# Performance work log

Hardware: AMD Instinct MI355X
Metric: run time of the kernel (lower is better)

The kernel has to match this reference:

```python
import jax, jax.numpy as jnp
import numpy as np

DIM = 1024
HID = 4096
NH = 16
HD = DIM // NH
B, S = 4, 2048
EPS = 1e-5
NEG = -1e9  # stand-in for -inf causal mask fill (numerically safe)


def layer_norm(x, g, b):
    mu = jnp.mean(x, axis=-1, keepdims=True)
    var = jnp.mean((x - mu) ** 2, axis=-1, keepdims=True)
    return (x - mu) * jax.lax.rsqrt(var + EPS) * g + b


def setup_inputs() -> dict:
    key = jax.random.key(0)
    ks = jax.random.split(key, 8)
    x = jax.random.normal(ks[0], (B, S, DIM), dtype=jnp.float32)
    # causal additive mask, broadcastable to [B, NH, S, S]
    causal = jnp.tril(jnp.ones((S, S), dtype=bool))
    mask = jnp.where(causal, 0.0, NEG).astype(jnp.float32)[None, None]
    sc = 1.0 / np.sqrt(DIM)
    wq = jax.random.normal(ks[1], (DIM, DIM), dtype=jnp.float32) * sc
    wk = jax.random.normal(ks[2], (DIM, DIM), dtype=jnp.float32) * sc
    wv = jax.random.normal(ks[3], (DIM, DIM), dtype=jnp.float32) * sc
    wo = jax.random.normal(ks[4], (DIM, DIM), dtype=jnp.float32) * sc
    w1 = jax.random.normal(ks[5], (DIM, HID), dtype=jnp.float32) * sc
    w2 = jax.random.normal(ks[6], (HID, DIM), dtype=jnp.float32) * (1.0 / np.sqrt(HID))
    ln1_w = jnp.ones((DIM,), jnp.float32); ln1_b = jnp.zeros((DIM,), jnp.float32)
    ln2_w = jnp.ones((DIM,), jnp.float32); ln2_b = jnp.zeros((DIM,), jnp.float32)
    return {"x": x, "mask": mask, "wq": wq, "wk": wk, "wv": wv, "wo": wo,
            "w1": w1, "w2": w2, "ln1_w": ln1_w, "ln1_b": ln1_b,
            "ln2_w": ln2_w, "ln2_b": ln2_b}


def reference(x, mask, wq, wk, wv, wo, w1, w2, ln1_w, ln1_b, ln2_w, ln2_b):
    b, s, _ = x.shape
    # pre-norm attention
    xn = layer_norm(x, ln1_w, ln1_b)
    q = (xn @ wq).reshape(b, s, NH, HD)
    k = (xn @ wk).reshape(b, s, NH, HD)
    v = (xn @ wv).reshape(b, s, NH, HD)
    scores = jnp.einsum('bqhd,bkhd->bhqk', q, k) / np.sqrt(HD) + mask
    probs = jax.nn.softmax(scores.astype(jnp.float32), axis=-1).astype(x.dtype)
    attn = jnp.einsum('bhqk,bkhd->bqhd', probs, v).reshape(b, s, NH * HD)
    h = x + attn @ wo
    # pre-norm ReLU FFN
    hn = layer_norm(h, ln2_w, ln2_b)
    ff = jax.nn.relu((hn @ w1).astype(jnp.float32)).astype(x.dtype) @ w2
    return h + ff
```

## Files before the change

kernel.cpp:

```cpp
#include <hip/hip_runtime.h>
#include <hip/hip_bf16.h>
#include <type_traits>

#define DIM 1024
#define HID 4096
#define NH 16
#define HD 64
#define BB 4
#define SS 2048
#define NROW (BB*SS)

typedef __attribute__((ext_vector_type(8))) short short8;
typedef __attribute__((ext_vector_type(4))) short short4v;
typedef __attribute__((ext_vector_type(4))) float f32x4;

__device__ __forceinline__ void gload16(const void* src, void* lds) {
  __builtin_amdgcn_global_load_lds(
      (const __attribute__((address_space(1))) unsigned int*)src,
      (__attribute__((address_space(3))) unsigned int*)lds, 16, 0, 0);
}
__device__ __forceinline__ short f2b(float f) {
  return __builtin_bit_cast(short, __float2bfloat16(f));
}
__device__ __forceinline__ float b2f(short s) {
  return __uint_as_float(((unsigned)(unsigned short)s) << 16);
}

__global__ __launch_bounds__(256) void ln_k(const float* __restrict__ x,
                                            const float* __restrict__ g,
                                            const float* __restrict__ bta,
                                            short* __restrict__ out) {
  int row = blockIdx.x;
  int t = threadIdx.x;
  int lane = t & 63, wid = t >> 6;
  float4 v = *(const float4*)(x + (size_t)row*DIM + t*4);
  float f[4] = {v.x, v.y, v.z, v.w};
  float s1 = 0.f, s2 = 0.f;
#pragma unroll
  for (int j = 0; j < 4; j++) { s1 += f[j]; s2 += f[j]*f[j]; }
#pragma unroll
  for (int off = 32; off > 0; off >>= 1) { s1 += __shfl_xor(s1, off); s2 += __shfl_xor(s2, off); }
  __shared__ float red[8];
  if (lane == 0) { red[wid] = s1; red[4+wid] = s2; }
  __syncthreads();
  s1 = red[0]+red[1]+red[2]+red[3];
  s2 = red[4]+red[5]+red[6]+red[7];
  float mu = s1 * (1.0f/DIM);
  float var = s2 * (1.0f/DIM) - mu*mu;
  float rs = rsqrtf(var + 1e-5f);
  float4 gv = *(const float4*)(g + t*4);
  float4 bv = *(const float4*)(bta + t*4);
  short4v o;
  o[0] = f2b((f[0]-mu)*rs*gv.x + bv.x);
  o[1] = f2b((f[1]-mu)*rs*gv.y + bv.y);
  o[2] = f2b((f[2]-mu)*rs*gv.z + bv.z);
  o[3] = f2b((f[3]-mu)*rs*gv.w + bv.w);
  *(short4v*)(out + (size_t)row*DIM + t*4) = o;
}

__global__ __launch_bounds__(256) void transp_f2b(const float* __restrict__ in, short* __restrict__ out,
                                                  int R, int C) {
  __shared__ __align__(16) short tile[64][72];
  int r0 = blockIdx.x*64, c0 = blockIdx.y*64;
  int t = threadIdx.x;
  int cr = t >> 4;
  int cc4 = (t & 15) * 4;
#pragma unroll
  for (int i = 0; i < 4; i++) {
    float4 v = *(const float4*)(in + (size_t)(r0 + cr + i*16)*C + c0 + cc4);
    tile[cr + i*16][cc4 + 0] = f2b(v.x);
    tile[cr + i*16][cc4 + 1] = f2b(v.y);
    tile[cr + i*16][cc4 + 2] = f2b(v.z);
    tile[cr + i*16][cc4 + 3] = f2b(v.w);
  }
  __syncthreads();
  int rr = t >> 3, cc = (t & 7) * 8;
#pragma unroll
  for (int i = 0; i < 2; i++) {
    int oc = rr + i*32;
    short8 v;
#pragma unroll
    for (int j = 0; j < 8; j++) v[j] = tile[cc + j][oc];
    *(short8*)(out + (size_t)(c0 + oc)*R + r0 + cc) = v;
  }
}

__global__ __launch_bounds__(256) void transp_f2b4(const float* __restrict__ w0, const float* __restrict__ w1,
                                                   const float* __restrict__ w2, const float* __restrict__ w3,
                                                   short* __restrict__ o0, short* __restrict__ o1,
                                                   short* __restrict__ o2, short* __restrict__ o3) {
  __shared__ __align__(16) short tile[64][72];
  int zz = blockIdx.z;
  const float* in = (zz == 0) ? w0 : (zz == 1) ? w1 : (zz == 2) ? w2 : w3;
  short* out = (zz == 0) ? o0 : (zz == 1) ? o1 : (zz == 2) ? o2 : o3;
  const int R = DIM, C = DIM;
  int r0 = blockIdx.x*64, c0 = blockIdx.y*64;
  int t = threadIdx.x;
  int cr = t >> 4;
  int cc4 = (t & 15) * 4;
#pragma unroll
  for (int i = 0; i < 4; i++) {
    float4 v = *(const float4*)(in + (size_t)(r0 + cr + i*16)*C + c0 + cc4);
    tile[cr + i*16][cc4 + 0] = f2b(v.x);
    tile[cr + i*16][cc4 + 1] = f2b(v.y);
    tile[cr + i*16][cc4 + 2] = f2b(v.z);
    tile[cr + i*16][cc4 + 3] = f2b(v.w);
  }
  __syncthreads();
  int rr = t >> 3, cc = (t & 7) * 8;
#pragma unroll
  for (int i = 0; i < 2; i++) {
    int oc = rr + i*32;
    short8 v;
#pragma unroll
    for (int j = 0; j < 8; j++) v[j] = tile[cc + j][oc];
    *(short8*)(out + (size_t)(c0 + oc)*R + r0 + cc) = v;
  }
}

__global__ __launch_bounds__(256) void vtrans(const short* __restrict__ qkv, short* __restrict__ vt) {
  __shared__ __align__(16) short tile[64][72];
  int s0 = blockIdx.x*64;
  int z = blockIdx.y; int b = z >> 4, h = z & 15;
  int t = threadIdx.x;
  int rr = t >> 3, cc = (t & 7) * 8;
#pragma unroll
  for (int i = 0; i < 2; i++) {
    short8 v = *(const short8*)(qkv + (size_t)(b*SS + s0 + rr + i*32)*(3*DIM) + 2*DIM + h*HD + cc);
    *(short8*)&tile[rr + i*32][cc] = v;
  }
  __syncthreads();
#pragma unroll
  for (int i = 0; i < 2; i++) {
    int d = rr + i*32;
    short8 v;
#pragma unroll
    for (int j = 0; j < 8; j++) v[j] = tile[cc + j][d];
    *(short8*)(vt + ((size_t)z*HD + d)*SS + s0 + cc) = v;
  }
}

template<int EPI, typename CT>
__global__ __launch_bounds__(512) void gemm_bt(const short* __restrict__ A, int lda,
                                               const short* __restrict__ Bt, int ldb,
                                               CT* C, int ldc,
                                               const float* Res, int ldr,
                                               int K) {
  __shared__ __align__(16) short ldsA[128*128];
  __shared__ __align__(16) short ldsB[128*128];
  int t = threadIdx.x, lane = t & 63, wid = t >> 6;
  int bm = blockIdx.x*128, bn = blockIdx.y*128;
  int wr = wid >> 2, wc = wid & 3;
  f32x4 z4 = {0.f, 0.f, 0.f, 0.f};
  f32x4 acc[4][2];
#pragma unroll
  for (int m = 0; m < 4; m++)
#pragma unroll
    for (int n = 0; n < 2; n++) acc[m][n] = z4;
  const int srcCol = (((t & 15) ^ ((t >> 4) & 15)) * 8);
  const short* pa = A + (size_t)(bm + (t >> 4))*lda + srcCol;
  const short* pb = Bt + (size_t)(bn + (t >> 4))*ldb + srcCol;
  const int rdXor = (lane & 15) << 3;
  for (int k0 = 0; k0 < K; k0 += 128) {
#pragma unroll
    for (int i = 0; i < 4; i++) {
      gload16(pa + (size_t)(i*32)*lda, &ldsA[i*4096 + wid*512]);
      gload16(pb + (size_t)(i*32)*ldb, &ldsB[i*4096 + wid*512]);
    }
    pa += 128; pb += 128;
    __syncthreads();
#pragma unroll
    for (int kk = 0; kk < 4; kk++) {
      short8 af[4], bfr[2];
#pragma unroll
      for (int m = 0; m < 4; m++) {
        int row = wr*64 + m*16 + (lane & 15);
        af[m] = *(const short8*)&ldsA[row*128 + ((kk*32 + (lane >> 4)*8) ^ rdXor)];
      }
#pragma unroll
      for (int n = 0; n < 2; n++) {
        int row = wc*32 + n*16 + (lane & 15);
        bfr[n] = *(const short8*)&ldsB[row*128 + ((kk*32 + (lane >> 4)*8) ^ rdXor)];
      }
#pragma unroll
      for (int m = 0; m < 4; m++)
#pragma unroll
        for (int n = 0; n < 2; n++)
          acc[m][n] = __builtin_amdgcn_mfma_f32_16x16x32_bf16(af[m], bfr[n], acc[m][n], 0, 0, 0);
    }
    __syncthreads();
  }
#pragma unroll
  for (int m = 0; m < 4; m++) {
    int r0 = bm + wr*64 + m*16 + ((lane >> 4) << 2);
#pragma unroll
    for (int n = 0; n < 2; n++) {
      int c = bn + wc*32 + n*16 + (lane & 15);
#pragma unroll
      for (int r = 0; r < 4; r++) {
        float v = acc[m][n][r];
        if constexpr (EPI == 1) v = fmaxf(v, 0.0f);
        if constexpr (EPI == 3) v += Res[(size_t)(r0 + r)*ldr + c];
        if constexpr (std::is_same<CT, float>::value)
          C[(size_t)(r0 + r)*ldc + c] = v;
        else
          C[(size_t)(r0 + r)*ldc + c] = f2b(v);
      }
    }
  }
}

__global__ __launch_bounds__(512) void attn_k(short* qkv, const short* __restrict__ vt) {
  __shared__ __align__(16) short ldsK[2][64*64];
  __shared__ __align__(16) short ldsV[2][64*64];
  __shared__ __align__(16) short ldsP[8][16*64];
  int t = threadIdx.x, lane = t & 63, wid = t >> 6;
  int wgid = blockIdx.x;
  int xcd = wgid & 7, idx = wgid >> 3;
  int z  = xcd*8 + (idx & 7);
  int p  = idx >> 3;
  int qiA = 15 - p, qiB = p;
  int b = z >> 4, h = z & 15;
  const int ld = 3*DIM;
  const float SCALE2 = 0.125f * 1.44269504f;
  const float THR2   = 8.0f * 1.44269504f;
  const int half = wid >> 2;
  const int nA = 2*qiA + 2;
  const int NT = 34;

  short8 qf[2];
  f32x4 z4 = {0.f, 0.f, 0.f, 0.f};
  f32x4 accO[4];
  float m_r[4], lp[4];
  const int srcCol = (((lane & 7) ^ ((lane >> 3) & 7)) * 8);
  const int rowXor = (lane & 7) << 3;

  auto LOADQ = [&](int q0) {
    const short* qp = qkv + (size_t)(b*SS + q0 + wid*16 + (lane & 15))*ld + h*HD + (lane >> 4)*8;
    qf[0] = *(const short8*)qp;
    qf[1] = *(const short8*)(qp + 32);
  };
  auto RESET = [&]() {
#pragma unroll
    for (int n = 0; n < 4; n++) accO[n] = z4;
#pragma unroll
    for (int r = 0; r < 4; r++) { m_r[r] = -1e30f; lp[r] = 0.f; }
  };
  auto EPILOG = [&](int q0e) {
    float rl[4];
#pragma unroll
    for (int r = 0; r < 4; r++) {
      float l = lp[r];
#pragma unroll
      for (int off = 1; off < 16; off <<= 1) l += __shfl_xor(l, off);
      rl[r] = 1.0f / l;
    }
#pragma unroll
    for (int nn = 0; nn < 4; nn++)
#pragma unroll
      for (int r = 0; r < 4; r++) {
        int qg = q0e + wid*16 + ((lane >> 4) << 2) + r;
        qkv[(size_t)(b*SS + qg)*ld + 2*DIM + h*HD + nn*16 + (lane & 15)] = f2b(accO[nn][r] * rl[r]);
      }
  };
  auto STAGE = [&](int kv0, int bsel) {
    const short* sk = qkv + (size_t)(b*SS + kv0 + (t >> 3))*ld + DIM + h*HD + srcCol;
    gload16(sk, &ldsK[bsel][wid*512]);
    const short* sv = vt + ((size_t)z*HD + (t >> 3))*SS + kv0 + srcCol;
    gload16(sv, &ldsV[bsel][wid*512]);
  };

  LOADQ(qiA*128);
  RESET();
  int qi = qiA, q0 = qiA*128;
  STAGE(0, 0);
  __syncthreads();
  for (int v = 0; v < NT; ++v) {
    int cur = v & 1;
    if (v + 1 < NT) {
      int vn = v + 1;
      STAGE(((vn >= nA) ? vn - nA : vn) * 64, cur ^ 1);
    }
    if (v == nA) {
      EPILOG(q0);
      RESET();
      qi = qiB; q0 = qiB*128;
      LOADQ(q0);
    }
    int it = (v >= nA) ? v - nA : v;
    int kv0 = it*64;
    if (it <= 2*qi + half) {
      f32x4 sacc[4];
#pragma unroll
      for (int n = 0; n < 4; n++) sacc[n] = z4;
      __builtin_amdgcn_s_setprio(1);
#pragma unroll
      for (int n = 0; n < 4; n++) {
#pragma unroll
        for (int kk = 0; kk < 2; kk++) {
          int colK = (kk*32 + (lane >> 4)*8) ^ rowXor;
          short8 kb = *(const short8*)&ldsK[cur][(n*16 + (lane & 15))*64 + colK];
          sacc[n] = __builtin_amdgcn_mfma_f32_16x16x32_bf16(qf[kk], kb, sacc[n], 0, 0, 0);
        }
      }
      __builtin_amdgcn_s_setprio(0);
      if (it == 2*qi + half) {
#pragma unroll
        for (int n = 0; n < 4; n++) {
          int kg = kv0 + n*16 + (lane & 15);
#pragma unroll
          for (int r = 0; r < 4; r++) {
            int qg = q0 + wid*16 + ((lane >> 4) << 2) + r;
            sacc[n][r] = (kg <= qg) ? sacc[n][r] : -1e30f;
          }
        }
      }
      float mxs[4];
      float dmax = -1e30f;
#pragma unroll
      for (int r = 0; r < 4; r++) {
        float mx = fmaxf(fmaxf(sacc[0][r], sacc[1][r]), fmaxf(sacc[2][r], sacc[3][r]));
#pragma unroll
        for (int off = 1; off < 16; off <<= 1) mx = fmaxf(mx, __shfl_xor(mx, off));
        mxs[r] = mx * SCALE2;
        dmax = fmaxf(dmax, mxs[r] - m_r[r]);
      }
      if (__any(dmax > THR2)) {
#pragma unroll
        for (int r = 0; r < 4; r++) {
          float mn = fmaxf(m_r[r], mxs[r]);
          float al = exp2f(m_r[r] - mn);
          m_r[r] = mn;
          lp[r] *= al;
#pragma unroll
          for (int n = 0; n < 4; n++) accO[n][r] *= al;
        }
      }
#pragma unroll
      for (int r = 0; r < 4; r++) {
        float mn = m_r[r];
        float rs = 0.f;
#pragma unroll
        for (int n = 0; n < 4; n++) {
          float p2 = exp2f(fmaf(sacc[n][r], SCALE2, -mn));
          sacc[n][r] = p2;
          rs += p2;
        }
        lp[r] += rs;
      }
#pragma unroll
      for (int n = 0; n < 4; n++)
#pragma unroll
        for (int r = 0; r < 4; r++) {
          int prow = ((lane >> 4) << 2) + r;
          int pcol = (n*16 + (lane & 15)) ^ ((prow & 7) << 3);
          ldsP[wid][prow*64 + pcol] = f2b(sacc[n][r]);
        }
      __builtin_amdgcn_s_setprio(1);
#pragma unroll
      for (int nn = 0; nn < 4; nn++) {
#pragma unroll
        for (int kk = 0; kk < 2; kk++) {
          int colP = (kk*32 + (lane >> 4)*8) ^ rowXor;
          short8 vb  = *(const short8*)&ldsV[cur][(nn*16 + (lane & 15))*64 + colP];
          short8 pfr = *(const short8*)&ldsP[wid][(lane & 15)*64 + colP];
          accO[nn] = __builtin_amdgcn_mfma_f32_16x16x32_bf16(pfr, vb, accO[nn], 0, 0, 0);
        }
      }
      __builtin_amdgcn_s_setprio(0);
    }
    __syncthreads();
  }
  EPILOG(q0);
}

extern "C" void kernel_launch(void* const* d_in, const int* in_sizes, int n_in,
                              void* d_out, int out_size, void* d_ws, size_t ws_size,
                              hipStream_t stream) {
  (void)in_sizes; (void)n_in; (void)out_size; (void)ws_size;
  const float* x    = (const float*)d_in[0];
  const float* wq   = (const float*)d_in[2];
  const float* wk   = (const float*)d_in[3];
  const float* wv   = (const float*)d_in[4];
  const float* wo   = (const float*)d_in[5];
  const float* w1   = (const float*)d_in[6];
  const float* w2   = (const float*)d_in[7];
  const float* ln1w = (const float*)d_in[8];
  const float* ln1b = (const float*)d_in[9];
  const float* ln2w = (const float*)d_in[10];
  const float* ln2b = (const float*)d_in[11];
  float* out = (float*)d_out;

  short* ws = (short*)d_ws;
  size_t o = 0;
  short* wqkvT = ws + o; o += (size_t)3*DIM*DIM;
  short* woT   = ws + o; o += (size_t)DIM*DIM;
  short* w1T   = ws + o; o += (size_t)HID*DIM;
  short* w2T   = ws + o; o += (size_t)DIM*HID;
  short* xn    = ws + o; o += (size_t)NROW*DIM;
  short* qkv   = ws + o; o += (size_t)NROW*3*DIM;
  short* ff1   = ws + o; o += (size_t)NROW*HID;
  short* vtb   = ff1;

  dim3 B256(256), B512(512);
  transp_f2b4<<<dim3(16,16,4), B256, 0, stream>>>(wq, wk, wv, wo,
                                                  wqkvT, wqkvT + DIM*DIM, wqkvT + 2*DIM*DIM, woT);
  transp_f2b<<<dim3(16,64), B256, 0, stream>>>(w1, w1T, DIM, HID);
  transp_f2b<<<dim3(64,16), B256, 0, stream>>>(w2, w2T, HID, DIM);
  ln_k<<<NROW, B256, 0, stream>>>(x, ln1w, ln1b, xn);
  gemm_bt<0, short><<<dim3(NROW/128, 3*DIM/128), B512, 0, stream>>>(xn, DIM, wqkvT, DIM, qkv, 3*DIM, nullptr, 0, DIM);
  vtrans<<<dim3(SS/64, BB*NH), B256, 0, stream>>>(qkv, vtb);
  attn_k<<<dim3(512), B512, 0, stream>>>(qkv, vtb);
  gemm_bt<3, float><<<dim3(NROW/128, DIM/128), B512, 0, stream>>>(qkv + 2*DIM, 3*DIM, woT, DIM, out, DIM, x, DIM, DIM);
  ln_k<<<NROW, B256, 0, stream>>>(out, ln2w, ln2b, xn);
  gemm_bt<1, short><<<dim3(NROW/128, HID/128), B512, 0, stream>>>(xn, DIM, w1T, DIM, ff1, HID, nullptr, 0, DIM);
  gemm_bt<3, float><<<dim3(NROW/128, DIM/128), B512, 0, stream>>>(ff1, HID, w2T, HID, out, DIM, out, DIM, HID);
}
```

Measured before the change: 385.0 us.

## Widen attention KV tile to 128 with per-wave diagonal causal masking

Doubles the KV block staged per iteration from 64 to 128 keys, halving the loop trip count and the number of block-wide barriers per query tile. All waves now process every KV block; on the diagonal block, waves skip QK MFMAs for sub-tiles fully above their rows and mask the rest. The V layout uses a 16-wide XOR swizzle for the 128-column rows, and P is written to LDS in two halves. This doubles K/V LDS footprint and register pressure for scores, which may reduce occupancy. Waves that previously skipped the second diagonal 64-block now do partly masked work.

```diff
diff --git a/kernel.cpp b/kernel.cpp
--- a/kernel.cpp
+++ b/kernel.cpp
@@ -211,8 +211,8 @@
 }
 
 __global__ __launch_bounds__(512) void attn_k(short* qkv, const short* __restrict__ vt) {
-  __shared__ __align__(16) short ldsK[2][64*64];
-  __shared__ __align__(16) short ldsV[2][64*64];
+  __shared__ __align__(16) short ldsK[2][128*64];
+  __shared__ __align__(16) short ldsV[2][64*128];
   __shared__ __align__(16) short ldsP[8][16*64];
   int t = threadIdx.x, lane = t & 63, wid = t >> 6;
   int wgid = blockIdx.x;
@@ -224,16 +224,17 @@
   const int ld = 3*DIM;
   const float SCALE2 = 0.125f * 1.44269504f;
   const float THR2   = 8.0f * 1.44269504f;
-  const int half = wid >> 2;
-  const int nA = 2*qiA + 2;
-  const int NT = 34;
+  const int nA = qiA + 1;
+  const int NT = 17;
 
   short8 qf[2];
   f32x4 z4 = {0.f, 0.f, 0.f, 0.f};
   f32x4 accO[4];
   float m_r[4], lp[4];
-  const int srcCol = (((lane & 7) ^ ((lane >> 3) & 7)) * 8);
-  const int rowXor = (lane & 7) << 3;
+  const int srcColK = (((t & 7) ^ ((t >> 3) & 7)) * 8);
+  const int srcColV = (((t & 15) ^ ((t >> 4) & 15)) * 8);
+  const int rowXor8  = (lane & 7) << 3;
+  const int rowXor16 = (lane & 15) << 3;
 
   auto LOADQ = [&](int q0) {
     const short* qp = qkv + (size_t)(b*SS + q0 + wid*16 + (lane & 15))*ld + h*HD + (lane >> 4)*8;
@@ -264,10 +265,12 @@
       }
   };
   auto STAGE = [&](int kv0, int bsel) {
-    const short* sk = qkv + (size_t)(b*SS + kv0 + (t >> 3))*ld + DIM + h*HD + srcCol;
-    gload16(sk, &ldsK[bsel][wid*512]);
-    const short* sv = vt + ((size_t)z*HD + (t >> 3))*SS + kv0 + srcCol;
-    gload16(sv, &ldsV[bsel][wid*512]);
+    const short* sk = qkv + (size_t)(b*SS + kv0 + (t >> 3))*ld + DIM + h*HD + srcColK;
+    gload16(sk,                 &ldsK[bsel][wid*512]);
+    gload16(sk + (size_t)64*ld, &ldsK[bsel][4096 + wid*512]);
+    const short* sv = vt + ((size_t)z*HD + (t >> 4))*SS + kv0 + srcColV;
+    gload16(sv,                 &ldsV[bsel][wid*512]);
+    gload16(sv + (size_t)32*SS, &ldsV[bsel][4096 + wid*512]);
   };
 
   LOADQ(qiA*128);
@@ -279,7 +282,7 @@
     int cur = v & 1;
     if (v + 1 < NT) {
       int vn = v + 1;
-      STAGE(((vn >= nA) ? vn - nA : vn) * 64, cur ^ 1);
+      STAGE(((vn >= nA) ? vn - nA : vn) * 128, cur ^ 1);
     }
     if (v == nA) {
       EPILOG(q0);
@@ -288,82 +291,96 @@
       LOADQ(q0);
     }
     int it = (v >= nA) ? v - nA : v;
-    int kv0 = it*64;
-    if (it <= 2*qi + half) {
-      f32x4 sacc[4];
-#pragma unroll
-      for (int n = 0; n < 4; n++) sacc[n] = z4;
-      __builtin_amdgcn_s_setprio(1);
-#pragma unroll
-      for (int n = 0; n < 4; n++) {
+    int kv0 = it*128;
+    bool diag = (it == qi);
+    f32x4 sacc[8];
+#pragma unroll
+    for (int n = 0; n < 8; n++) sacc[n] = z4;
+    __builtin_amdgcn_s_setprio(1);
+#pragma unroll
+    for (int n = 0; n < 8; n++) {
+      if (!diag || n <= wid) {
 #pragma unroll
         for (int kk = 0; kk < 2; kk++) {
-          int colK = (kk*32 + (lane >> 4)*8) ^ rowXor;
+          int colK = (kk*32 + (lane >> 4)*8) ^ rowXor8;
           short8 kb = *(const short8*)&ldsK[cur][(n*16 + (lane & 15))*64 + colK];
           sacc[n] = __builtin_amdgcn_mfma_f32_16x16x32_bf16(qf[kk], kb, sacc[n], 0, 0, 0);
         }
       }
-      __builtin_amdgcn_s_setprio(0);
-      if (it == 2*qi + half) {
-#pragma unroll
-        for (int n = 0; n < 4; n++) {
+    }
+    __builtin_amdgcn_s_setprio(0);
+    if (diag) {
+#pragma unroll
+      for (int n = 0; n < 8; n++) {
+        if (n == wid) {
           int kg = kv0 + n*16 + (lane & 15);
 #pragma unroll
           for (int r = 0; r < 4; r++) {
             int qg = q0 + wid*16 + ((lane >> 4) << 2) + r;
             sacc[n][r] = (kg <= qg) ? sacc[n][r] : -1e30f;
           }
+        } else if (n > wid) {
+#pragma unroll
+          for (int r = 0; r < 4; r++) sacc[n][r] = -1e30f;
         }
       }
-      float mxs[4];
-      float dmax = -1e30f;
+    }
+    float mxs[4];
+    float dmax = -1e30f;
+#pragma unroll
+    for (int r = 0; r < 4; r++) {
+      float m01 = fmaxf(sacc[0][r], sacc[1][r]);
+      float m23 = fmaxf(sacc[2][r], sacc[3][r]);
+      float m45 = fmaxf(sacc[4][r], sacc[5][r]);
+      float m67 = fmaxf(sacc[6][r], sacc[7][r]);
+      float mx = fmaxf(fmaxf(m01, m23), fmaxf(m45, m67));
+#pragma unroll
+      for (int off = 1; off < 16; off <<= 1) mx = fmaxf(mx, __shfl_xor(mx, off));
+      mxs[r] = mx * SCALE2;
+      dmax = fmaxf(dmax, mxs[r] - m_r[r]);
+    }
+    if (__any(dmax > THR2)) {
 #pragma unroll
       for (int r = 0; r < 4; r++) {
-        float mx = fmaxf(fmaxf(sacc[0][r], sacc[1][r]), fmaxf(sacc[2][r], sacc[3][r]));
-#pragma unroll
-        for (int off = 1; off < 16; off <<= 1) mx = fmaxf(mx, __shfl_xor(mx, off));
-        mxs[r] = mx * SCALE2;
-        dmax = fmaxf(dmax, mxs[r] - m_r[r]);
-      }
-      if (__any(dmax > THR2)) {
-#pragma unroll
-        for (int r = 0; r < 4; r++) {
-          float mn = fmaxf(m_r[r], mxs[r]);
-          float al = exp2f(m_r[r] - mn);
-          m_r[r] = mn;
-          lp[r] *= al;
-#pragma unroll
-          for (int n = 0; n < 4; n++) accO[n][r] *= al;
-        }
-      }
-#pragma unroll
-      for (int r = 0; r < 4; r++) {
-        float mn = m_r[r];
-        float rs = 0.f;
-#pragma unroll
-        for (int n = 0; n < 4; n++) {
-          float p2 = exp2f(fmaf(sacc[n][r], SCALE2, -mn));
-          sacc[n][r] = p2;
-          rs += p2;
-        }
-        lp[r] += rs;
-      }
-#pragma unroll
-      for (int n = 0; n < 4; n++)
+        float mn = fmaxf(m_r[r], mxs[r]);
+        float al = exp2f(m_r[r] - mn);
+        m_r[r] = mn;
+        lp[r] *= al;
+#pragma unroll
+        for (int n = 0; n < 4; n++) accO[n][r] *= al;
+      }
+    }
+#pragma unroll
+    for (int r = 0; r < 4; r++) {
+      float mn = m_r[r];
+      float rs = 0.f;
+#pragma unroll
+      for (int n = 0; n < 8; n++) {
+        float p2 = exp2f(fmaf(sacc[n][r], SCALE2, -mn));
+        sacc[n][r] = p2;
+        rs += p2;
+      }
+      lp[r] += rs;
+    }
+#pragma unroll
+    for (int hh = 0; hh < 2; hh++) {
+#pragma unroll
+      for (int j = 0; j < 4; j++)
 #pragma unroll
         for (int r = 0; r < 4; r++) {
           int prow = ((lane >> 4) << 2) + r;
-          int pcol = (n*16 + (lane & 15)) ^ ((prow & 7) << 3);
-          ldsP[wid][prow*64 + pcol] = f2b(sacc[n][r]);
+          int pcol = (j*16 + (lane & 15)) ^ ((prow & 7) << 3);
+          ldsP[wid][prow*64 + pcol] = f2b(sacc[hh*4 + j][r]);
         }
       __builtin_amdgcn_s_setprio(1);
 #pragma unroll
       for (int nn = 0; nn < 4; nn++) {
 #pragma unroll
-        for (int kk = 0; kk < 2; kk++) {
-          int colP = (kk*32 + (lane >> 4)*8) ^ rowXor;
-          short8 vb  = *(const short8*)&ldsV[cur][(nn*16 + (lane & 15))*64 + colP];
+        for (int kk2 = 0; kk2 < 2; kk2++) {
+          int colP = (kk2*32 + (lane >> 4)*8) ^ rowXor8;
           short8 pfr = *(const short8*)&ldsP[wid][(lane & 15)*64 + colP];
+          int colV = ((hh*2 + kk2)*32 + (lane >> 4)*8) ^ rowXor16;
+          short8 vb = *(const short8*)&ldsV[cur][(nn*16 + (lane & 15))*128 + colV];
           accO[nn] = __builtin_amdgcn_mfma_f32_16x16x32_bf16(pfr, vb, accO[nn], 0, 0, 0);
         }
       }
```

Result: no change. 380.5 us (-1.2%).
